# Kernel tuning notes

Hardware: AMD Instinct MI355X
Metric: run time of the kernel (lower is better)

The kernel has to match this reference:

```python
import jax, jax.numpy as jnp
import numpy as np

_CLAMP = 1e6  # clamp bound for real/imag parts after each eml level
CPLX = jnp.complex64


def _eml_op(u, v):
    # eml(u, v) = exp(log(u) * log(v)) in complex arithmetic
    return jnp.exp(jnp.log(u) * jnp.log(v))


def _sanitize(z):
    r = jnp.clip(jnp.nan_to_num(z.real, nan=0.0, posinf=_CLAMP, neginf=-_CLAMP), -_CLAMP, _CLAMP)
    i = jnp.clip(jnp.nan_to_num(z.imag, nan=0.0, posinf=_CLAMP, neginf=-_CLAMP), -_CLAMP, _CLAMP)
    return jax.lax.complex(r, i)


def setup_inputs() -> dict:
    key = jax.random.key(0)
    k1, k2, k3 = jax.random.split(key, 3)
    depth = 10
    n_leaves = 2 ** depth          # 1024
    n_internal = n_leaves - 1      # 1023
    init_scale = 0.1
    batch = 65536
    x = jax.random.normal(k1, (batch,), jnp.float32)
    leaf = jax.random.normal(k2, (n_leaves, 2), jnp.float32) * init_scale
    leaf = leaf.at[:, 0].add(1.0)  # leaf_init[:, 0] += 1.0
    gate = jax.random.normal(k3, (n_internal, 2, 3), jnp.float32) * init_scale
    gate = gate.at[..., 2].add(1.0)  # gate_init[..., 2] += 1.0
    return {"x": x, "leaf_logits": leaf, "gate_logits": gate}


def reference(x, leaf_logits, gate_logits):
    xc = x.astype(CPLX)                      # [B]
    a = leaf_logits[:, 0].astype(CPLX)       # [L]
    b = leaf_logits[:, 1].astype(CPLX)       # [L]
    level = a[None, :] + b[None, :] * xc[:, None]   # [B, L] leaf inputs: alpha + beta*x
    x_b = xc[:, None]                        # [B, 1]
    g_all = gate_logits.astype(CPLX)         # [L-1, 2, 3]
    node_idx = 0
    while level.shape[1] > 1:
        n_pairs = level.shape[1] // 2
        left = level[:, 0::2]                # [B, n_pairs]
        right = level[:, 1::2]
        g = g_all[node_idx:node_idx + n_pairs]
        left_in = g[:, 0, 0][None] + g[:, 0, 1][None] * x_b + g[:, 0, 2][None] * left
        right_in = g[:, 1, 0][None] + g[:, 1, 1][None] * x_b + g[:, 1, 2][None] * right
        level = _sanitize(_eml_op(left_in, right_in))
        node_idx += n_pairs
    return level[:, 0]                       # [B] complex64
```

## Files before the change

### kernel.cpp

```cpp
#include <hip/hip_runtime.h>
#include <math.h>

#define CLAMPV 1000000.0f
#define PI_F     3.14159274f
#define HALFPI_F 1.57079633f
#define LN2_F    0.69314718f
#define L2E_F    1.44269504f
#define C1_F     0.17328680f
#define C2_F     0.05515890f
#define C2R_F    0.11031780f

typedef float v2f __attribute__((ext_vector_type(2)));

__device__ __forceinline__ v2f vb(float s) { return (v2f){s, s}; }
__device__ __forceinline__ v2f vfma(v2f a, v2f b, v2f c) { return __builtin_elementwise_fma(a, b, c); }

__device__ __forceinline__ const float* gptr(const float* __restrict__ g, int node) {
    return g + 6 * __builtin_amdgcn_readfirstlane(node);
}

__device__ __forceinline__ v2f sanitv(v2f v) {
    v2f c;
    c.x = __builtin_amdgcn_fmed3f(v.x, -CLAMPV, CLAMPV);
    c.y = __builtin_amdgcn_fmed3f(v.y, -CLAMPV, CLAMPV);
    c.x = (v.x != v.x) ? 0.0f : c.x;
    c.y = (v.y != v.y) ? 0.0f : c.y;
    return c;
}

__device__ __forceinline__ v2f fatan2v(v2f y, v2f x) {
    v2f ax = __builtin_elementwise_abs(x);
    v2f ay = __builtin_elementwise_abs(y);
    v2f mx = __builtin_elementwise_max(ax, ay);
    v2f mn = __builtin_elementwise_min(ax, ay);
    v2f r  = (v2f){__builtin_amdgcn_rcpf(mx.x), __builtin_amdgcn_rcpf(mx.y)};
    v2f t  = mn * r;
    v2f z  = t * t;
    v2f p  = vfma(z, vfma(z, vfma(z, vfma(z,
             vb(0.02083510f), vb(-0.08513300f)), vb(0.18014100f)), vb(-0.33029950f)),
             vb(0.99986600f));
    p = p * t;
    p.x = (ay.x > ax.x) ? (HALFPI_F - p.x) : p.x;
    p.y = (ay.y > ax.y) ? (HALFPI_F - p.y) : p.y;
    p.x = (x.x < 0.0f) ? (PI_F - p.x) : p.x;
    p.y = (x.y < 0.0f) ? (PI_F - p.y) : p.y;
    p.x = copysignf(p.x, y.x);
    p.y = copysignf(p.y, y.y);
    return p;
}

__device__ __forceinline__ void exp_tailv(v2f e, v2f f0, v2f& ore, v2f& oim) {
    v2f r = (v2f){__builtin_amdgcn_exp2f(e.x), __builtin_amdgcn_exp2f(e.y)};
    v2f f = (v2f){__builtin_amdgcn_fractf(f0.x), __builtin_amdgcn_fractf(f0.y)};
    v2f sn = (v2f){__builtin_amdgcn_sinf(f.x), __builtin_amdgcn_sinf(f.y)};
    v2f cs = (v2f){__builtin_amdgcn_cosf(f.x), __builtin_amdgcn_cosf(f.y)};
    ore = sanitv(r * cs);
    oim = sanitv(r * sn);
}

__device__ __forceinline__ void fast_rp(v2f ure, v2f vre, v2f& ore, v2f& oim) {
    v2f L2u = (v2f){__builtin_amdgcn_logf(ure.x), __builtin_amdgcn_logf(ure.y)};
    v2f L2v = (v2f){__builtin_amdgcn_logf(vre.x), __builtin_amdgcn_logf(vre.y)};
    v2f e = (vb(LN2_F) * L2u) * L2v;
    v2f r = (v2f){__builtin_amdgcn_exp2f(e.x), __builtin_amdgcn_exp2f(e.y)};
    v2f c = __builtin_elementwise_min(r, vb(CLAMPV));
    c.x = (r.x != r.x) ? 0.0f : c.x;
    c.y = (r.y != r.y) ? 0.0f : c.y;
    ore = c;
    oim = vb(0.0f);
}

__device__ __forceinline__ void node_any(
    v2f lre, v2f lim, v2f rre, v2f rim,
    v2f x, const float* __restrict__ g,
    v2f& ore, v2f& oim)
{
    float g0 = g[0], g1 = g[1], g2 = g[2], g3 = g[3], g4 = g[4], g5 = g[5];
    v2f ure = vfma(vb(g2), lre, vfma(vb(g1), x, vb(g0)));
    v2f vre = vfma(vb(g5), rre, vfma(vb(g4), x, vb(g3)));
    v2f mn = __builtin_elementwise_min(ure, vre);

    unsigned long long bad =
        __ballot(lim.x != 0.0f) | __ballot(lim.y != 0.0f) |
        __ballot(rim.x != 0.0f) | __ballot(rim.y != 0.0f) |
        __ballot(mn.x <= 0.0f)  | __ballot(mn.y <= 0.0f);

    if (bad == 0ULL) {
        fast_rp(ure, vre, ore, oim);
    } else {
        v2f uim = vfma(vb(g2), lim, vb(0.0f));
        v2f vim = vfma(vb(g5), rim, vb(0.0f));

        v2f nu = vfma(ure, ure, uim * uim);
        v2f nv = vfma(vre, vre, vim * vim);
        v2f L2u = (v2f){__builtin_amdgcn_logf(nu.x), __builtin_amdgcn_logf(nu.y)};
        v2f L2v = (v2f){__builtin_amdgcn_logf(nv.x), __builtin_amdgcn_logf(nv.y)};
        v2f Au = fatan2v(uim, ure);
        v2f Av = fatan2v(vim, vre);

        v2f t2 = vb(L2E_F) * (Au * Av);
        v2f e  = vfma(vb(C1_F) * L2u, L2v, -t2);
        v2f s2 = vfma(L2u, Av, Au * L2v);
        v2f f0 = vb(C2_F) * s2;
        exp_tailv(e, f0, ore, oim);
    }
}

__device__ __forceinline__ void node_r0(
    v2f l, v2f r, v2f x, const float* __restrict__ g,
    v2f& ore, v2f& oim)
{
    float g0 = g[0], g1 = g[1], g2 = g[2], g3 = g[3], g4 = g[4], g5 = g[5];
    v2f u = vfma(vb(g2), l, vfma(vb(g1), x, vb(g0)));
    v2f v = vfma(vb(g5), r, vfma(vb(g4), x, vb(g3)));
    v2f mn = __builtin_elementwise_min(u, v);

    unsigned long long bad = __ballot(mn.x <= 0.0f) | __ballot(mn.y <= 0.0f);

    if (bad == 0ULL) {
        fast_rp(u, v, ore, oim);
    } else {
        v2f au = __builtin_elementwise_abs(u);
        v2f av = __builtin_elementwise_abs(v);
        v2f L2u = (v2f){__builtin_amdgcn_logf(au.x), __builtin_amdgcn_logf(au.y)};
        v2f L2v = (v2f){__builtin_amdgcn_logf(av.x), __builtin_amdgcn_logf(av.y)};
        v2f Au, Av;
        Au.x = (u.x < 0.0f) ? PI_F : 0.0f;
        Au.y = (u.y < 0.0f) ? PI_F : 0.0f;
        Av.x = (v.x < 0.0f) ? PI_F : 0.0f;
        Av.y = (v.y < 0.0f) ? PI_F : 0.0f;

        v2f t2 = vb(L2E_F) * (Au * Av);
        v2f e  = vfma(vb(LN2_F) * L2u, L2v, -t2);
        v2f s2 = vfma(L2u, Av, Au * L2v);
        v2f f0 = vb(C2R_F) * s2;
        exp_tailv(e, f0, ore, oim);
    }
}

__global__ __launch_bounds__(1024, 8) void EMLTree1DLinear_kernel(
    const float* __restrict__ x_g,
    const float* __restrict__ leaf_g,
    const float* __restrict__ gate_g,
    float* __restrict__ out,
    int batch, int out_real_only)
{
    __shared__ float4 s_t[16][64];

    const int lane = threadIdx.x;
    const int s    = threadIdx.y;

    const int e0 = blockIdx.x * 128 + lane;
    const v2f x2 = (v2f){x_g[e0], x_g[e0 + 64]};

    v2f cAre, cAim, cBre, cBim, rootre, rootim;

#pragma clang loop unroll(disable)
    for (int q = 0; q < 4; ++q) {
        const int jq = 64 * s + 16 * q;
        v2f r2re[2], r2im[2];
        v2f h1re = vb(0.0f), h1im = vb(0.0f);
        v2f cre, cim;

#pragma unroll
        for (int p = 0; p < 4; ++p) {
            const int j = jq + 4 * p;
            const float* L = leaf_g + 2 * __builtin_amdgcn_readfirstlane(j);
            v2f l0 = vfma(vb(L[1]), x2, vb(L[0]));
            v2f l1 = vfma(vb(L[3]), x2, vb(L[2]));
            v2f l2 = vfma(vb(L[5]), x2, vb(L[4]));
            v2f l3 = vfma(vb(L[7]), x2, vb(L[6]));

            v2f Are, Aim, Bre, Bim;
            node_r0(l0, l1, x2, gptr(gate_g, j >> 1), Are, Aim);
            node_r0(l2, l3, x2, gptr(gate_g, (j >> 1) + 1), Bre, Bim);

            v2f r1re, r1im;
            node_any(Are, Aim, Bre, Bim, x2, gptr(gate_g, 512 + (j >> 2)), r1re, r1im);

            if (p & 1) {
                node_any(h1re, h1im, r1re, r1im, x2,
                         gptr(gate_g, 768 + (j >> 3)), r2re[p >> 1], r2im[p >> 1]);
            } else {
                h1re = r1re; h1im = r1im;
            }
        }
        node_any(r2re[0], r2im[0], r2re[1], r2im[1], x2,
                 gptr(gate_g, 896 + (jq >> 4)), cre, cim);

        if (q == 0) {
            cAre = cre; cAim = cim;
        } else if (q == 1) {
            node_any(cAre, cAim, cre, cim, x2, gptr(gate_g, 960 + 2 * s), cBre, cBim);
        } else if (q == 2) {
            cAre = cre; cAim = cim;
        } else {
            v2f tre, tim;
            node_any(cAre, cAim, cre, cim, x2, gptr(gate_g, 961 + 2 * s), tre, tim);
            node_any(cBre, cBim, tre, tim, x2, gptr(gate_g, 992 + s), rootre, rootim);
        }
    }

    s_t[s][lane] = make_float4(rootre.x, rootre.y, rootim.x, rootim.y);
    __syncthreads();
    if (s != 0) return;

#pragma clang loop unroll(disable)
    for (int L = 6; L <= 9; ++L) {
        const int cnt  = 1 << (9 - L);
        const int base = 1024 - (1 << (10 - L));
#pragma clang loop unroll(disable)
        for (int j = 0; j < cnt; ++j) {
            float4 a = s_t[2 * j][lane], b = s_t[2 * j + 1][lane];
            v2f rre, rim;
            node_any((v2f){a.x, a.y}, (v2f){a.z, a.w},
                     (v2f){b.x, b.y}, (v2f){b.z, b.w},
                     x2, gptr(gate_g, base + j), rre, rim);
            s_t[j][lane] = make_float4(rre.x, rre.y, rim.x, rim.y);
        }
    }

    float4 fin = s_t[0][lane];
    if (out_real_only) {
        out[e0]      = fin.x;
        out[e0 + 64] = fin.y;
    } else {
        reinterpret_cast<float2*>(out)[e0]      = make_float2(fin.x, fin.z);
        reinterpret_cast<float2*>(out)[e0 + 64] = make_float2(fin.y, fin.w);
    }
}

extern "C" void kernel_launch(void* const* d_in, const int* in_sizes, int n_in,
                              void* d_out, int out_size, void* d_ws, size_t ws_size,
                              hipStream_t stream) {
    const float* x    = (const float*)d_in[0];
    const float* leaf = (const float*)d_in[1];
    const float* gate = (const float*)d_in[2];
    float* out = (float*)d_out;
    const int batch = in_sizes[0];

    const int out_real_only = (out_size == batch) ? 1 : 0;

    dim3 block(64, 16);
    dim3 grid(batch / 128);
    hipLaunchKernelGGL(EMLTree1DLinear_kernel, grid, block, 0, stream,
                       x, leaf, gate, out, batch, out_real_only);
}
```

Measured before the change: 113.9 us.

## Bucket-sort inputs by value before tree evaluation to reduce wavefront divergence

Adds a histogram, scan and scatter pass that groups batch elements by the top bits of their order-preserving float key. The main kernel then reads the sorted x values and scatters results back through the stored index. Neighbouring lanes then see similar x, which is meant to make branch and sign-dependent paths in the node evaluation uniform across each wavefront. The cost is four extra small kernel launches, global atomics, and uncoalesced output writes. It only runs when the workspace is large enough.

```diff
diff --git a/kernel.cpp b/kernel.cpp
--- a/kernel.cpp
+++ b/kernel.cpp
@@ -10,6 +10,8 @@
 #define C2_F     0.05515890f
 #define C2R_F    0.11031780f
 
+#define NBIN 4096
+
 typedef float v2f __attribute__((ext_vector_type(2)));
 
 __device__ __forceinline__ v2f vb(float s) { return (v2f){s, s}; }
@@ -17,6 +19,12 @@
 
 __device__ __forceinline__ const float* gptr(const float* __restrict__ g, int node) {
     return g + 6 * __builtin_amdgcn_readfirstlane(node);
+}
+
+__device__ __forceinline__ unsigned sortkey(float x) {
+    unsigned u = __float_as_uint(x);
+    u ^= (unsigned)(((int)u) >> 31) | 0x80000000u;
+    return u;
 }
 
 __device__ __forceinline__ v2f sanitv(v2f v) {
@@ -138,10 +146,53 @@
     }
 }
 
+
+__global__ void eml_zero_hist(unsigned* __restrict__ hist) {
+    hist[blockIdx.x * 1024 + threadIdx.x] = 0u;
+}
+
+__global__ void eml_hist(const float* __restrict__ x, unsigned* __restrict__ hist, int n) {
+    int i = blockIdx.x * 1024 + threadIdx.x;
+    if (i < n) atomicAdd(&hist[sortkey(x[i]) >> 20], 1u);
+}
+
+__global__ void eml_scan(const unsigned* __restrict__ hist, unsigned* __restrict__ offs) {
+    __shared__ unsigned part[1024];
+    int t = threadIdx.x;
+    unsigned h0 = hist[4*t], h1 = hist[4*t+1], h2 = hist[4*t+2], h3 = hist[4*t+3];
+    unsigned sum = h0 + h1 + h2 + h3;
+    part[t] = sum;
+    __syncthreads();
+    for (int d = 1; d < 1024; d <<= 1) {
+        unsigned v = (t >= d) ? part[t - d] : 0u;
+        __syncthreads();
+        part[t] += v;
+        __syncthreads();
+    }
+    unsigned excl = part[t] - sum;
+    offs[4*t]   = excl;
+    offs[4*t+1] = excl + h0;
+    offs[4*t+2] = excl + h0 + h1;
+    offs[4*t+3] = excl + h0 + h1 + h2;
+}
+
+__global__ void eml_scatter(const float* __restrict__ x, unsigned* __restrict__ offs,
+                            unsigned* __restrict__ sidx, float* __restrict__ xs, int n) {
+    int i = blockIdx.x * 1024 + threadIdx.x;
+    if (i < n) {
+        float xv = x[i];
+        unsigned pos = atomicAdd(&offs[sortkey(xv) >> 20], 1u);
+        sidx[pos] = (unsigned)i;
+        xs[pos]   = xv;
+    }
+}
+
 __global__ __launch_bounds__(1024, 8) void EMLTree1DLinear_kernel(
     const float* __restrict__ x_g,
     const float* __restrict__ leaf_g,
     const float* __restrict__ gate_g,
+    const unsigned* __restrict__ sidx,
+    const float* __restrict__ xs,
     float* __restrict__ out,
     int batch, int out_real_only)
 {
@@ -150,8 +201,9 @@
     const int lane = threadIdx.x;
     const int s    = threadIdx.y;
 
-    const int e0 = blockIdx.x * 128 + lane;
-    const v2f x2 = (v2f){x_g[e0], x_g[e0 + 64]};
+    const int p0 = blockIdx.x * 128 + lane;
+    const v2f x2 = sidx ? (v2f){xs[p0], xs[p0 + 64]}
+                        : (v2f){x_g[p0], x_g[p0 + 64]};
 
     v2f cAre, cAim, cBre, cBim, rootre, rootim;
 
@@ -221,12 +273,14 @@
     }
 
     float4 fin = s_t[0][lane];
+    const int i0 = sidx ? (int)sidx[p0]      : p0;
+    const int i1 = sidx ? (int)sidx[p0 + 64] : p0 + 64;
     if (out_real_only) {
-        out[e0]      = fin.x;
-        out[e0 + 64] = fin.y;
+        out[i0] = fin.x;
+        out[i1] = fin.y;
     } else {
-        reinterpret_cast<float2*>(out)[e0]      = make_float2(fin.x, fin.z);
-        reinterpret_cast<float2*>(out)[e0 + 64] = make_float2(fin.y, fin.w);
+        reinterpret_cast<float2*>(out)[i0] = make_float2(fin.x, fin.z);
+        reinterpret_cast<float2*>(out)[i1] = make_float2(fin.y, fin.w);
     }
 }
 
@@ -241,8 +295,28 @@
 
     const int out_real_only = (out_size == batch) ? 1 : 0;
 
+    const size_t need = (size_t)NBIN * 4 * 2 + (size_t)batch * 4 * 2;
+    unsigned* hist = (unsigned*)d_ws;
+    unsigned* offs = hist + NBIN;
+    unsigned* sidx = offs + NBIN;
+    float*    xs   = (float*)(sidx + batch);
+
+    const bool use_sort = (ws_size >= need) && (batch % 128 == 0);
+
+    if (use_sort) {
+        hipLaunchKernelGGL(eml_zero_hist, dim3(NBIN / 1024), dim3(1024), 0, stream, hist);
+        hipLaunchKernelGGL(eml_hist, dim3((batch + 1023) / 1024), dim3(1024), 0, stream,
+                           x, hist, batch);
+        hipLaunchKernelGGL(eml_scan, dim3(1), dim3(1024), 0, stream, hist, offs);
+        hipLaunchKernelGGL(eml_scatter, dim3((batch + 1023) / 1024), dim3(1024), 0, stream,
+                           x, offs, sidx, xs, batch);
+    }
+
     dim3 block(64, 16);
     dim3 grid(batch / 128);
     hipLaunchKernelGGL(EMLTree1DLinear_kernel, grid, block, 0, stream,
-                       x, leaf, gate, out, batch, out_real_only);
-}
+                       x, leaf, gate,
+                       use_sort ? sidx : (const unsigned*)nullptr,
+                       use_sort ? xs : (const float*)nullptr,
+                       out, batch, out_real_only);
+}
```

Measured after the change: 246.7 us. 117% more time.

## Add real-only fast path with taint tracking and compacted complex fallback

Applied to the files above, without the earlier changes.

Splits evaluation into two kernels. The first evaluates the tree with real-only arithmetic (log2/exp2 on positive values) and tracks the minimum node input. Elements where every input stayed positive are written directly; the rest are compacted via ballot/atomic into a workspace list. A second kernel runs the full complex path only on listed elements and exits early for blocks beyond the count. This adds a memset, a second launch and an atomic, and in exchange avoids the complex atan2/sincos work for elements that never go negative.

```diff
diff --git a/kernel.cpp b/kernel.cpp
--- a/kernel.cpp
+++ b/kernel.cpp
@@ -18,6 +18,110 @@
 __device__ __forceinline__ const float* gptr(const float* __restrict__ g, int node) {
     return g + 6 * __builtin_amdgcn_readfirstlane(node);
 }
+
+__device__ __forceinline__ unsigned rank_below(unsigned long long m) {
+    return __builtin_amdgcn_mbcnt_hi((unsigned)(m >> 32),
+           __builtin_amdgcn_mbcnt_lo((unsigned)m, 0u));
+}
+
+__device__ __forceinline__ v2f fnode(v2f l, v2f r, v2f x,
+                                     const float* __restrict__ g, v2f& tmin) {
+    float g0 = g[0], g1 = g[1], g2 = g[2], g3 = g[3], g4 = g[4], g5 = g[5];
+    v2f u = vfma(vb(g2), l, vfma(vb(g1), x, vb(g0)));
+    v2f v = vfma(vb(g5), r, vfma(vb(g4), x, vb(g3)));
+    tmin = __builtin_elementwise_min(tmin, __builtin_elementwise_min(u, v));
+    v2f L2u = (v2f){__builtin_amdgcn_logf(u.x), __builtin_amdgcn_logf(u.y)};
+    v2f L2v = (v2f){__builtin_amdgcn_logf(v.x), __builtin_amdgcn_logf(v.y)};
+    v2f e = (vb(LN2_F) * L2u) * L2v;
+    v2f rr = (v2f){__builtin_amdgcn_exp2f(e.x), __builtin_amdgcn_exp2f(e.y)};
+    return __builtin_elementwise_min(rr, vb(CLAMPV));
+}
+
+__global__ __launch_bounds__(1024, 8) void eml_fast_taint(
+    const float* __restrict__ x_g, const float* __restrict__ leaf_g,
+    const float* __restrict__ gate_g, float* __restrict__ out,
+    unsigned* __restrict__ cnt, unsigned* __restrict__ list,
+    int batch, int out_real_only)
+{
+    __shared__ float4 s_t[16][64];
+
+    const int lane = threadIdx.x;
+    const int s    = threadIdx.y;
+    const int e0 = blockIdx.x * 128 + lane;
+    const v2f x2 = (v2f){x_g[e0], x_g[e0 + 64]};
+
+    v2f tmin = vb(1.0f);
+    v2f cA, cB, root;
+
+#pragma clang loop unroll(disable)
+    for (int q = 0; q < 4; ++q) {
+        const int jq = 64 * s + 16 * q;
+        v2f r2[2], h1, c;
+#pragma unroll
+        for (int p = 0; p < 4; ++p) {
+            const int j = jq + 4 * p;
+            const float* L = leaf_g + 2 * __builtin_amdgcn_readfirstlane(j);
+            v2f l0 = vfma(vb(L[1]), x2, vb(L[0]));
+            v2f l1 = vfma(vb(L[3]), x2, vb(L[2]));
+            v2f l2 = vfma(vb(L[5]), x2, vb(L[4]));
+            v2f l3 = vfma(vb(L[7]), x2, vb(L[6]));
+
+            v2f A  = fnode(l0, l1, x2, gptr(gate_g, j >> 1), tmin);
+            v2f B  = fnode(l2, l3, x2, gptr(gate_g, (j >> 1) + 1), tmin);
+            v2f r1 = fnode(A, B, x2, gptr(gate_g, 512 + (j >> 2)), tmin);
+            if (p & 1) r2[p >> 1] = fnode(h1, r1, x2, gptr(gate_g, 768 + (j >> 3)), tmin);
+            else       h1 = r1;
+        }
+        c = fnode(r2[0], r2[1], x2, gptr(gate_g, 896 + (jq >> 4)), tmin);
+        if      (q == 0) cA = c;
+        else if (q == 1) cB = fnode(cA, c, x2, gptr(gate_g, 960 + 2 * s), tmin);
+        else if (q == 2) cA = c;
+        else {
+            v2f t = fnode(cA, c, x2, gptr(gate_g, 961 + 2 * s), tmin);
+            root  = fnode(cB, t, x2, gptr(gate_g, 992 + s), tmin);
+        }
+    }
+
+    s_t[s][lane] = make_float4(root.x, root.y, tmin.x, tmin.y);
+    __syncthreads();
+    if (s != 0) return;
+
+#pragma clang loop unroll(disable)
+    for (int L = 6; L <= 9; ++L) {
+        const int cntL = 1 << (9 - L);
+        const int base = 1024 - (1 << (10 - L));
+#pragma clang loop unroll(disable)
+        for (int j = 0; j < cntL; ++j) {
+            float4 a = s_t[2 * j][lane], b = s_t[2 * j + 1][lane];
+            v2f tm = __builtin_elementwise_min((v2f){a.z, a.w}, (v2f){b.z, b.w});
+            v2f r  = fnode((v2f){a.x, a.y}, (v2f){b.x, b.y}, x2,
+                           gptr(gate_g, base + j), tm);
+            s_t[j][lane] = make_float4(r.x, r.y, tm.x, tm.y);
+        }
+    }
+
+    float4 fin = s_t[0][lane];
+    const bool t0 = !(fin.z > 0.0f);
+    const bool t1 = !(fin.w > 0.0f);
+
+    if (!t0) {
+        if (out_real_only) out[e0] = fin.x;
+        else reinterpret_cast<float2*>(out)[e0] = make_float2(fin.x, 0.0f);
+    }
+    if (!t1) {
+        if (out_real_only) out[e0 + 64] = fin.y;
+        else reinterpret_cast<float2*>(out)[e0 + 64] = make_float2(fin.y, 0.0f);
+    }
+
+    unsigned long long m0 = __ballot(t0), m1 = __ballot(t1);
+    int n0 = __popcll(m0), n1 = __popcll(m1);
+    unsigned base = 0;
+    if (lane == 0 && (n0 + n1)) base = atomicAdd(cnt, (unsigned)(n0 + n1));
+    base = __shfl(base, 0);
+    if (t0) list[base + rank_below(m0)] = (unsigned)e0;
+    if (t1) list[base + n0 + rank_below(m1)] = (unsigned)(e0 + 64);
+}
+
 
 __device__ __forceinline__ v2f sanitv(v2f v) {
     v2f c;
@@ -138,20 +242,24 @@
     }
 }
 
-__global__ __launch_bounds__(1024, 8) void EMLTree1DLinear_kernel(
-    const float* __restrict__ x_g,
-    const float* __restrict__ leaf_g,
-    const float* __restrict__ gate_g,
-    float* __restrict__ out,
+__global__ __launch_bounds__(1024, 8) void eml_slow(
+    const float* __restrict__ x_g, const float* __restrict__ leaf_g,
+    const float* __restrict__ gate_g, const unsigned* __restrict__ cnt,
+    const unsigned* __restrict__ list, float* __restrict__ out,
     int batch, int out_real_only)
 {
     __shared__ float4 s_t[16][64];
 
+    const unsigned count = cnt[0];
+    const unsigned r0 = blockIdx.x * 128u;
+    if (r0 >= count) return;
+
     const int lane = threadIdx.x;
     const int s    = threadIdx.y;
-
-    const int e0 = blockIdx.x * 128 + lane;
-    const v2f x2 = (v2f){x_g[e0], x_g[e0 + 64]};
+    const unsigned ra = min(r0 + (unsigned)lane, count - 1u);
+    const unsigned rb = min(r0 + (unsigned)lane + 64u, count - 1u);
+    const unsigned ia = list[ra], ib = list[rb];
+    const v2f x2 = (v2f){x_g[ia], x_g[ib]};
 
     v2f cAre, cAim, cBre, cBim, rootre, rootim;
 
@@ -185,8 +293,10 @@
                 h1re = r1re; h1im = r1im;
             }
         }
+        v2f cre2, cim2;
         node_any(r2re[0], r2im[0], r2re[1], r2im[1], x2,
-                 gptr(gate_g, 896 + (jq >> 4)), cre, cim);
+                 gptr(gate_g, 896 + (jq >> 4)), cre2, cim2);
+        cre = cre2; cim = cim2;
 
         if (q == 0) {
             cAre = cre; cAim = cim;
@@ -207,10 +317,10 @@
 
 #pragma clang loop unroll(disable)
     for (int L = 6; L <= 9; ++L) {
-        const int cnt  = 1 << (9 - L);
+        const int cntL = 1 << (9 - L);
         const int base = 1024 - (1 << (10 - L));
 #pragma clang loop unroll(disable)
-        for (int j = 0; j < cnt; ++j) {
+        for (int j = 0; j < cntL; ++j) {
             float4 a = s_t[2 * j][lane], b = s_t[2 * j + 1][lane];
             v2f rre, rim;
             node_any((v2f){a.x, a.y}, (v2f){a.z, a.w},
@@ -222,11 +332,11 @@
 
     float4 fin = s_t[0][lane];
     if (out_real_only) {
-        out[e0]      = fin.x;
-        out[e0 + 64] = fin.y;
+        out[ia] = fin.x;
+        out[ib] = fin.y;
     } else {
-        reinterpret_cast<float2*>(out)[e0]      = make_float2(fin.x, fin.z);
-        reinterpret_cast<float2*>(out)[e0 + 64] = make_float2(fin.y, fin.w);
+        reinterpret_cast<float2*>(out)[ia] = make_float2(fin.x, fin.z);
+        reinterpret_cast<float2*>(out)[ib] = make_float2(fin.y, fin.w);
     }
 }
 
@@ -241,8 +351,15 @@
 
     const int out_real_only = (out_size == batch) ? 1 : 0;
 
+    unsigned* cnt  = (unsigned*)d_ws;
+    unsigned* list = (unsigned*)d_ws + 64;
+
+    hipMemsetAsync(cnt, 0, sizeof(unsigned), stream);
+
     dim3 block(64, 16);
     dim3 grid(batch / 128);
-    hipLaunchKernelGGL(EMLTree1DLinear_kernel, grid, block, 0, stream,
-                       x, leaf, gate, out, batch, out_real_only);
-}
+    hipLaunchKernelGGL(eml_fast_taint, grid, block, 0, stream,
+                       x, leaf, gate, out, cnt, list, batch, out_real_only);
+    hipLaunchKernelGGL(eml_slow, grid, block, 0, stream,
+                       x, leaf, gate, cnt, list, out, batch, out_real_only);
+}
```

Result: slower. 128.8 us (+13.1%).
